# Optimization experiments

Hardware: AMD Instinct MI355X
Metric: run time of the kernel (lower is better)

Reference implementation:

```python
import jax, jax.numpy as jnp
import numpy as np

GRID_H, GRID_W, INPUT_DIM = 256, 256, 64
BATCH = 4096


def setup_inputs() -> dict:
    key = jax.random.key(0)
    k_in, k_w = jax.random.split(key)
    inputs = jax.random.uniform(k_in, (BATCH, INPUT_DIM), dtype=jnp.float32)
    # SOM weights initialized uniform[0,1) as in the original layer
    weights_map = jax.random.uniform(k_w, (GRID_H, GRID_W, INPUT_DIM), dtype=jnp.float32)
    return {"inputs": inputs, "weights_map": weights_map}


def reference(inputs, weights_map):
    """Inference forward of SOM2dLayer: find BMU coords + quantization error.

    inputs:      [B, D]
    weights_map: [H, W, D]
    returns (bmu_indices [B,2] int32, quantization_errors [B] float32)
    """
    H, W, D = weights_map.shape
    flat_w = weights_map.reshape(H * W, D)            # [N, D]
    x2 = jnp.sum(inputs * inputs, axis=1, keepdims=True)      # [B, 1]
    w2 = jnp.sum(flat_w * flat_w, axis=1)                     # [N]
    d2 = x2 - 2.0 * (inputs @ flat_w.T) + w2                  # [B, N]
    d2 = jnp.maximum(d2, 0.0)                                 # numerical floor
    bmu_flat = jnp.argmin(d2, axis=1)                         # [B]
    bmu_y = (bmu_flat // W).astype(jnp.int32)
    bmu_x = (bmu_flat % W).astype(jnp.int32)
    bmu_indices = jnp.stack([bmu_y, bmu_x], axis=1)           # [B, 2]
    min_d2 = jnp.take_along_axis(d2, bmu_flat[:, None], axis=1)[:, 0]
    quantization_errors = jnp.sqrt(min_d2)                    # [B]
    return bmu_indices, quantization_errors
```

## Files before the change

kernel.cpp:

```cpp
#include <hip/hip_runtime.h>
#include <math.h>


typedef short  bf16x8 __attribute__((ext_vector_type(8)));
typedef float  f32x4  __attribute__((ext_vector_type(4)));
typedef unsigned short u16;
typedef unsigned short u16x4 __attribute__((ext_vector_type(4)));

constexpr int D     = 64;
constexpr int NW    = 65536;
constexpr int B     = 4096;
constexpr int NSUB  = 256;
constexpr int NFINE = NW / 16;
constexpr float MARG_HALF = 0.15f;

constexpr int STRIPS   = 32;
constexpr int STRIP_N  = NW / STRIPS;
constexpr int PANELS   = 8;
constexpr int ROWS_BLK = 128;

__device__ inline u16 bf16u(float f) {
    union { float f; unsigned u; } v; v.f = f;
    unsigned b = v.u;
    b += 0x7fffu + ((b >> 16) & 1u);
    return (u16)(b >> 16);
}

__device__ inline u16 bf16up(float f) {
    union { float f; unsigned u; } v; v.f = f;
    unsigned h = v.u >> 16;
    if ((v.u & 0xFFFFu) && !(v.u >> 31)) h += 1;
    return (u16)h;
}

__device__ __forceinline__ void gload_lds16(const void* g, void* l) {
    __builtin_amdgcn_global_load_lds(
        (const __attribute__((address_space(1))) unsigned int*)g,
        (__attribute__((address_space(3))) unsigned int*)l, 16, 0, 0);
}

__global__ __launch_bounds__(256) void k_prep(const float* __restrict__ w,
                                              const float* __restrict__ x,
                                              u16* __restrict__ whi,
                                              u16* __restrict__ xhi,
                                              float* __restrict__ w2c) {
    const int idx = blockIdx.x * 256 + threadIdx.x;
    if (idx < NW) {
        const float4* wr = reinterpret_cast<const float4*>(w + (size_t)idx * D);
        u16* orow = whi + (size_t)idx * D;
        float a0 = 0.f, a1 = 0.f, a2 = 0.f, a3 = 0.f;
#pragma unroll
        for (int h = 0; h < 8; ++h) {
            float4 v0 = wr[2 * h], v1 = wr[2 * h + 1];
            a0 = fmaf(v0.x, v0.x, a0); a1 = fmaf(v0.y, v0.y, a1);
            a2 = fmaf(v0.z, v0.z, a2); a3 = fmaf(v0.w, v0.w, a3);
            a0 = fmaf(v1.x, v1.x, a0); a1 = fmaf(v1.y, v1.y, a1);
            a2 = fmaf(v1.z, v1.z, a2); a3 = fmaf(v1.w, v1.w, a3);
            bf16x8 o = {(short)bf16u(v0.x), (short)bf16u(v0.y),
                        (short)bf16u(v0.z), (short)bf16u(v0.w),
                        (short)bf16u(v1.x), (short)bf16u(v1.y),
                        (short)bf16u(v1.z), (short)bf16u(v1.w)};
            *reinterpret_cast<bf16x8*>(orow + 8 * h) = o;
        }
        w2c[idx] = -0.5f * ((a0 + a1) + (a2 + a3));
    } else {
        const int r = idx - NW;
        const float4* xr = reinterpret_cast<const float4*>(x + (size_t)r * D);
        u16* orow = xhi + (size_t)r * D;
#pragma unroll
        for (int h = 0; h < 8; ++h) {
            float4 v0 = xr[2 * h], v1 = xr[2 * h + 1];
            bf16x8 o = {(short)bf16u(v0.x), (short)bf16u(v0.y),
                        (short)bf16u(v0.z), (short)bf16u(v0.w),
                        (short)bf16u(v1.x), (short)bf16u(v1.y),
                        (short)bf16u(v1.z), (short)bf16u(v1.w)};
            *reinterpret_cast<bf16x8*>(orow + 8 * h) = o;
        }
    }
}

template <int WRITE_FINE>
__global__ __launch_bounds__(256, 2) void k_screen0(
        const u16* __restrict__ whi, const u16* __restrict__ xhi,
        const float* __restrict__ w2c, float* __restrict__ pm,
        u16* __restrict__ pmf) {
    __shared__ __align__(16) char smem[32768];
    const int bid   = blockIdx.x;
    const int strip = bid & 31;
    const int rbk   = bid >> 5;
    const int tid   = threadIdx.x;
    const int wv    = tid >> 6;
    const int lane  = tid & 63;
    const int col   = lane & 15;
    const int kg    = lane >> 4;
    const int row0  = rbk * ROWS_BLK;

    bf16x8 a[8][2];
#pragma unroll
    for (int rg = 0; rg < 8; ++rg)
#pragma unroll
        for (int h = 0; h < 2; ++h)
            a[rg][h] = *reinterpret_cast<const bf16x8*>(
                xhi + (size_t)(row0 + rg * 16 + col) * D + h * 32 + kg * 8);

    const char* wbase = (const char*)whi + (size_t)strip * STRIP_N * 128;
    unsigned soff[8];
#pragma unroll
    for (int i = 0; i < 8; ++i) {
        unsigned o = (unsigned)(i * 256 + tid) * 16;
        soff[i] = o ^ (((o >> 7) & 7u) << 4);
    }

    const unsigned msk = (unsigned)(col & 7) << 4;
    const float* w2s = w2c + strip * STRIP_N;

    float mx[8][4];
#pragma unroll
    for (int rg = 0; rg < 8; ++rg)
#pragma unroll
        for (int r = 0; r < 4; ++r) mx[rg][r] = -3.4e38f;

    for (int p = 0; p < PANELS; ++p) {
#pragma unroll
        for (int i = 0; i < 8; ++i)
            gload_lds16(wbase + (size_t)p * 32768 + soff[i],
                        &smem[i * 4096 + wv * 1024]);
        __syncthreads();

        const float* w2p = w2s + p * 256;
#pragma unroll
        for (int t = 0; t < 4; ++t) {
            const int nloc = wv * 64 + t * 16 + col;
            const unsigned u0 = (unsigned)nloc * 128 + kg * 16;
            const bf16x8 b0 = *reinterpret_cast<const bf16x8*>(smem + (u0 ^ msk));
            const bf16x8 b1 = *reinterpret_cast<const bf16x8*>(smem + ((u0 + 64) ^ msk));
            const float c = w2p[nloc];
            const f32x4 cq = {c, c, c, c};
#pragma unroll
            for (int rg = 0; rg < 8; ++rg) {
                f32x4 acc = __builtin_amdgcn_mfma_f32_16x16x32_bf16(a[rg][0], b0, cq, 0, 0, 0);
                acc = __builtin_amdgcn_mfma_f32_16x16x32_bf16(a[rg][1], b1, acc, 0, 0, 0);
                mx[rg][0] = fmaxf(mx[rg][0], acc[0]);
                mx[rg][1] = fmaxf(mx[rg][1], acc[1]);
                mx[rg][2] = fmaxf(mx[rg][2], acc[2]);
                mx[rg][3] = fmaxf(mx[rg][3], acc[3]);
            }
        }

        if ((p & 3) == 3) {
            const int s = strip * 8 + (p >> 2) * 4 + wv;

            if (WRITE_FINE) {
                const int f = s * 16 + col;
#pragma unroll
                for (int rg = 0; rg < 8; ++rg) {
                    u16x4 h4 = {bf16up(mx[rg][0]), bf16up(mx[rg][1]),
                                bf16up(mx[rg][2]), bf16up(mx[rg][3])};
                    *reinterpret_cast<u16x4*>(
                        pmf + (size_t)f * B + row0 + rg * 16 + kg * 4) = h4;
                }
            }

#pragma unroll
            for (int rg = 0; rg < 8; ++rg) {
                float v0 = mx[rg][0], v1 = mx[rg][1], v2 = mx[rg][2], v3 = mx[rg][3];
#pragma unroll
                for (int sh = 1; sh < 16; sh <<= 1) {
                    v0 = fmaxf(v0, __shfl_xor(v0, sh, 64));
                    v1 = fmaxf(v1, __shfl_xor(v1, sh, 64));
                    v2 = fmaxf(v2, __shfl_xor(v2, sh, 64));
                    v3 = fmaxf(v3, __shfl_xor(v3, sh, 64));
                }
                float vv = v0;
                vv = (col == 1) ? v1 : vv;
                vv = (col == 2) ? v2 : vv;
                vv = (col == 3) ? v3 : vv;
                if (col < 4)
                    pm[(size_t)(row0 + rg * 16 + kg * 4 + col) * NSUB + s] = vv;
                mx[rg][0] = -3.4e38f; mx[rg][1] = -3.4e38f;
                mx[rg][2] = -3.4e38f; mx[rg][3] = -3.4e38f;
            }
        }
        __syncthreads();
    }
}

template <int FINE>
__global__ __launch_bounds__(256) void k_rescore(
        const float* __restrict__ x, const float* __restrict__ w,
        const float* __restrict__ w2c, const float* __restrict__ pm,
        const u16* __restrict__ pmf, float* __restrict__ out) {
    const int wv   = threadIdx.x >> 6;
    const int lane = threadIdx.x & 63;
    const int row  = blockIdx.x * 4 + wv;

    float pv[4];
#pragma unroll
    for (int it = 0; it < 4; ++it)
        pv[it] = pm[(size_t)row * NSUB + it * 64 + lane];
    float gm = fmaxf(fmaxf(pv[0], pv[1]), fmaxf(pv[2], pv[3]));
#pragma unroll
    for (int s = 1; s < 64; s <<= 1) gm = fmaxf(gm, __shfl_xor(gm, s, 64));
    const float thr = gm - MARG_HALF;

    const float4* xr = reinterpret_cast<const float4*>(x + (size_t)row * D);
    float4 xq[16];
#pragma unroll
    for (int q = 0; q < 16; ++q) xq[q] = xr[q];

    float bestv = 3.4e38f;
    int   besti = 0x7fffffff;

#pragma unroll
    for (int it = 0; it < 4; ++it) {
        unsigned long long bm = __ballot(pv[it] >= thr);
        while (bm) {
            int sb = __ffsll(bm) - 1;
            bm &= bm - 1;
            int sub  = it * 64 + sb;
            int base = (sub >> 3) * 2048 + ((sub >> 2) & 1) * 1024 + (sub & 3) * 64;

            if (FINE) {
                float fv = -3.4e38f;
                if (lane < 16) {
                    union { unsigned u; float f; } c;
                    c.u = (unsigned)pmf[(size_t)(sub * 16 + lane) * B + row] << 16;
                    fv = c.f;
                }
                unsigned long long fm = __ballot(fv >= thr);
                while (fm) {
                    int colq = __ffsll(fm) - 1;
                    fm &= fm - 1;
                    int j = lane & 15, q = lane >> 4;
                    int n = base + (j >> 2) * 256 + (j & 3) * 16 + colq;
                    const float4* wr = reinterpret_cast<const float4*>(w + (size_t)n * D);
                    float d0 = 0.f, d1 = 0.f, d2 = 0.f, d3 = 0.f;
#pragma unroll
                    for (int k = 0; k < 4; ++k) {
                        float4 wq = wr[q * 4 + k];
                        float4 xv = xq[q * 4 + k];
                        d0 = fmaf(xv.x, wq.x, d0); d1 = fmaf(xv.y, wq.y, d1);
                        d2 = fmaf(xv.z, wq.z, d2); d3 = fmaf(xv.w, wq.w, d3);
                    }
                    float d = (d0 + d1) + (d2 + d3);
                    d += __shfl_xor(d, 16, 64);
                    d += __shfl_xor(d, 32, 64);
                    float val = -2.f * (d + w2c[n]);
                    if (val < bestv || (val == bestv && n < besti)) { bestv = val; besti = n; }
                }
            } else {
#pragma unroll
                for (int p4 = 0; p4 < 4; ++p4) {
                    int n = base + p4 * 256 + lane;
                    const float4* wr = reinterpret_cast<const float4*>(w + (size_t)n * D);
                    float d0 = 0.f, d1 = 0.f, d2 = 0.f, d3 = 0.f;
#pragma unroll
                    for (int q = 0; q < 16; ++q) {
                        float4 wq = wr[q];
                        d0 = fmaf(xq[q].x, wq.x, d0);
                        d1 = fmaf(xq[q].y, wq.y, d1);
                        d2 = fmaf(xq[q].z, wq.z, d2);
                        d3 = fmaf(xq[q].w, wq.w, d3);
                    }
                    float dot = (d0 + d1) + (d2 + d3);
                    float val = -2.f * (dot + w2c[n]);
                    if (val < bestv || (val == bestv && n < besti)) { bestv = val; besti = n; }
                }
            }
        }
    }
#pragma unroll
    for (int s = 1; s < 64; s <<= 1) {
        float ov = __shfl_xor(bestv, s, 64);
        int   oi = __shfl_xor(besti, s, 64);
        if (ov < bestv || (ov == bestv && oi < besti)) { bestv = ov; besti = oi; }
    }
    if (lane == 0) {
        float a0 = 0.f, a1 = 0.f, a2 = 0.f, a3 = 0.f;
#pragma unroll
        for (int q = 0; q < 16; ++q) {
            a0 = fmaf(xq[q].x, xq[q].x, a0);
            a1 = fmaf(xq[q].y, xq[q].y, a1);
            a2 = fmaf(xq[q].z, xq[q].z, a2);
            a3 = fmaf(xq[q].w, xq[q].w, a3);
        }
        float x2 = (a0 + a1) + (a2 + a3);
        float d2f = x2 + bestv;
        if (d2f < 0.f) d2f = 0.f;
        out[row * 2 + 0] = (float)(besti >> 8);
        out[row * 2 + 1] = (float)(besti & 255);
        out[2 * B + row] = sqrtf(d2f);
    }
}

__global__ __launch_bounds__(256) void fb_w2(const float* __restrict__ w,
                                             float* __restrict__ w2) {
    int n = blockIdx.x * 256 + threadIdx.x;
    const float4* wr = reinterpret_cast<const float4*>(w + (size_t)n * D);
    float a0 = 0.f, a1 = 0.f, a2 = 0.f, a3 = 0.f;
#pragma unroll
    for (int q = 0; q < 16; ++q) {
        float4 v = wr[q];
        a0 = fmaf(v.x, v.x, a0); a1 = fmaf(v.y, v.y, a1);
        a2 = fmaf(v.z, v.z, a2); a3 = fmaf(v.w, v.w, a3);
    }
    w2[n] = (a0 + a1) + (a2 + a3);
}

__global__ __launch_bounds__(256) void fb_main(const float* __restrict__ x,
                                               const float* __restrict__ w,
                                               const float* __restrict__ w2,
                                               float* __restrict__ ps,
                                               int* __restrict__ pi) {
    constexpr int NSTRIP = NW / 32;
    const int rb    = blockIdx.x & 15;
    const int strip = blockIdx.x >> 4;
    const int row   = rb * 256 + threadIdx.x;
    float xr[D];
    const float4* xrow = reinterpret_cast<const float4*>(x + (size_t)row * D);
#pragma unroll
    for (int q = 0; q < 16; ++q) {
        float4 v = xrow[q];
        xr[q * 4 + 0] = v.x; xr[q * 4 + 1] = v.y;
        xr[q * 4 + 2] = v.z; xr[q * 4 + 3] = v.w;
    }
    float best = 3.4e38f; int bidx = 0;
    const int n0 = strip * NSTRIP, n1 = n0 + NSTRIP;
    for (int n = n0; n < n1; ++n) {
        const float* wr = w + (size_t)n * D;
        float a0 = 0.f, a1 = 0.f, a2 = 0.f, a3 = 0.f;
#pragma unroll
        for (int d = 0; d < D; d += 4) {
            a0 = fmaf(xr[d + 0], wr[d + 0], a0);
            a1 = fmaf(xr[d + 1], wr[d + 1], a1);
            a2 = fmaf(xr[d + 2], wr[d + 2], a2);
            a3 = fmaf(xr[d + 3], wr[d + 3], a3);
        }
        float s = fmaf(-2.f, (a0 + a1) + (a2 + a3), w2[n]);
        if (s < best) { best = s; bidx = n; }
    }
    ps[(size_t)strip * B + row] = best;
    pi[(size_t)strip * B + row] = bidx;
}

__global__ __launch_bounds__(256) void fb_merge(const float* __restrict__ x,
                                                const float* __restrict__ ps,
                                                const int* __restrict__ pi,
                                                float* __restrict__ out) {
    int row = blockIdx.x * 256 + threadIdx.x;
    float bs = 3.5e38f; int bi = 0;
    for (int t = 0; t < 32; ++t) {
        float s = ps[(size_t)t * B + row];
        int   i = pi[(size_t)t * B + row];
        if (s < bs || (s == bs && i < bi)) { bs = s; bi = i; }
    }
    const float4* xrow = reinterpret_cast<const float4*>(x + (size_t)row * D);
    float a0 = 0.f, a1 = 0.f, a2 = 0.f, a3 = 0.f;
#pragma unroll
    for (int q = 0; q < 16; ++q) {
        float4 v = xrow[q];
        a0 = fmaf(v.x, v.x, a0); a1 = fmaf(v.y, v.y, a1);
        a2 = fmaf(v.z, v.z, a2); a3 = fmaf(v.w, v.w, a3);
    }
    float x2 = (a0 + a1) + (a2 + a3);
    float d2 = x2 + bs;
    if (d2 < 0.f) d2 = 0.f;
    out[row * 2 + 0] = (float)(bi >> 8);
    out[row * 2 + 1] = (float)(bi & 255);
    out[2 * B + row] = sqrtf(d2);
}

extern "C" void kernel_launch(void* const* d_in, const int* in_sizes, int n_in,
                              void* d_out, int out_size, void* d_ws, size_t ws_size,
                              hipStream_t stream) {
    const float* x = (const float*)d_in[0];
    const float* w = (const float*)d_in[1];
    float* out = (float*)d_out;

    const size_t whi_sz = (size_t)NW * D * 2;
    const size_t xhi_sz = (size_t)B * D * 2;
    const size_t w2c_sz = (size_t)NW * 4;
    const size_t pm_sz  = (size_t)B * NSUB * 4;
    const size_t pmf_sz = (size_t)NFINE * B * 2;
    const size_t need_c = whi_sz + xhi_sz + w2c_sz + pm_sz;
    const size_t need_f = need_c + pmf_sz;

    if (ws_size >= need_c) {
        char* p = (char*)d_ws;
        u16*   whi = (u16*)p;   p += whi_sz;
        u16*   xhi = (u16*)p;   p += xhi_sz;
        float* w2c = (float*)p; p += w2c_sz;
        float* pm  = (float*)p; p += pm_sz;
        u16*   pmf = (u16*)p;

        k_prep<<<(NW + B) / 256, 256, 0, stream>>>(w, x, whi, xhi, w2c);
        if (ws_size >= need_f) {
            k_screen0<1><<<STRIPS * (B / ROWS_BLK), 256, 0, stream>>>(whi, xhi, w2c, pm, pmf);
            k_rescore<1><<<B / 4, 256, 0, stream>>>(x, w, w2c, pm, pmf, out);
        } else {
            k_screen0<0><<<STRIPS * (B / ROWS_BLK), 256, 0, stream>>>(whi, xhi, w2c, pm, pmf);
            k_rescore<0><<<B / 4, 256, 0, stream>>>(x, w, w2c, pm, pmf, out);
        }
    } else {
        float* w2 = (float*)d_ws;
        float* ps = w2 + NW;
        int*   pi = (int*)(ps + (size_t)32 * B);
        fb_w2<<<NW / 256, 256, 0, stream>>>(w, w2);
        fb_main<<<16 * 32, 256, 0, stream>>>(x, w, w2, ps, pi);
        fb_merge<<<B / 256, 256, 0, stream>>>(x, ps, pi, out);
    }
}
```

Baseline: 124.7 us.

## Stage screen outputs in shared memory and write pmf/pm as contiguous tiles

The screening kernel now stages its per-subcell fine maxima and coarse maxima in shared memory, then writes them out as contiguous 16-byte chunks. The fine-score buffer is re-laid out as [sub][row-block][row][16], so each block's tile is one contiguous 4 KB region. The rescore kernel reads that buffer with the matching new indexing, which gives 16 contiguous u16s per row instead of a stride-B gather. This targets scattered, narrow global stores and strided reads, at the cost of two extra __syncthreads per flush and shared-memory bank traffic.

```diff
diff --git a/kernel.cpp b/kernel.cpp
--- a/kernel.cpp
+++ b/kernel.cpp
@@ -5,7 +5,6 @@
 typedef short  bf16x8 __attribute__((ext_vector_type(8)));
 typedef float  f32x4  __attribute__((ext_vector_type(4)));
 typedef unsigned short u16;
-typedef unsigned short u16x4 __attribute__((ext_vector_type(4)));
 
 constexpr int D     = 64;
 constexpr int NW    = 65536;
@@ -85,6 +84,7 @@
         const float* __restrict__ w2c, float* __restrict__ pm,
         u16* __restrict__ pmf) {
     __shared__ __align__(16) char smem[32768];
+    __shared__ __align__(16) float pmsh[512];
     const int bid   = blockIdx.x;
     const int strip = bid & 31;
     const int rbk   = bid >> 5;
@@ -148,17 +148,19 @@
         }
 
         if ((p & 3) == 3) {
-            const int s = strip * 8 + (p >> 2) * 4 + wv;
+            const int s0 = strip * 8 + (p >> 2) * 4;
+            const int s  = s0 + wv;
+
+            __syncthreads();
 
             if (WRITE_FINE) {
-                const int f = s * 16 + col;
-#pragma unroll
-                for (int rg = 0; rg < 8; ++rg) {
-                    u16x4 h4 = {bf16up(mx[rg][0]), bf16up(mx[rg][1]),
-                                bf16up(mx[rg][2]), bf16up(mx[rg][3])};
-                    *reinterpret_cast<u16x4*>(
-                        pmf + (size_t)f * B + row0 + rg * 16 + kg * 4) = h4;
-                }
+                u16* st = reinterpret_cast<u16*>(smem);
+#pragma unroll
+                for (int rg = 0; rg < 8; ++rg)
+#pragma unroll
+                    for (int r = 0; r < 4; ++r)
+                        st[wv * 2048 + (rg * 16 + kg * 4 + r) * 16 + col] =
+                            bf16up(mx[rg][r]);
             }
 
 #pragma unroll
@@ -176,9 +178,24 @@
                 vv = (col == 2) ? v2 : vv;
                 vv = (col == 3) ? v3 : vv;
                 if (col < 4)
-                    pm[(size_t)(row0 + rg * 16 + kg * 4 + col) * NSUB + s] = vv;
+                    pmsh[(rg * 16 + kg * 4 + col) * 4 + wv] = vv;
                 mx[rg][0] = -3.4e38f; mx[rg][1] = -3.4e38f;
                 mx[rg][2] = -3.4e38f; mx[rg][3] = -3.4e38f;
+            }
+
+            __syncthreads();
+
+            if (WRITE_FINE) {
+                const char* src = smem + wv * 4096;
+                char* dstg = (char*)pmf + ((size_t)s * 32 + rbk) * 4096;
+#pragma unroll
+                for (int i = 0; i < 4; ++i)
+                    *reinterpret_cast<float4*>(dstg + i * 1024 + lane * 16) =
+                        *reinterpret_cast<const float4*>(src + i * 1024 + lane * 16);
+            }
+            if (tid < 128) {
+                float4 v = *reinterpret_cast<const float4*>(&pmsh[tid * 4]);
+                *reinterpret_cast<float4*>(&pm[(size_t)(row0 + tid) * NSUB + s0]) = v;
             }
         }
         __syncthreads();
@@ -193,6 +210,8 @@
     const int wv   = threadIdx.x >> 6;
     const int lane = threadIdx.x & 63;
     const int row  = blockIdx.x * 4 + wv;
+    const int rbk2 = row >> 7;
+    const int rl   = row & 127;
 
     float pv[4];
 #pragma unroll
@@ -224,7 +243,8 @@
                 float fv = -3.4e38f;
                 if (lane < 16) {
                     union { unsigned u; float f; } c;
-                    c.u = (unsigned)pmf[(size_t)(sub * 16 + lane) * B + row] << 16;
+                    c.u = (unsigned)pmf[((size_t)sub * 32 + rbk2) * 2048
+                                        + rl * 16 + lane] << 16;
                     fv = c.f;
                 }
                 unsigned long long fm = __ballot(fv >= thr);
```

After: 113.4 us. 1.1x faster.
